# Performance work log

Measured on AMD Instinct MI355X. Metric: run time of the kernel, lower is better.

Reference implementation:

```python
import jax, jax.numpy as jnp
import numpy as np

B, T, P, H = 32, 4096, 512, 512  # batch, frames, phonemes, hidden


def setup_inputs() -> dict:
    key = jax.random.key(0)
    ks = jax.random.split(key, 10)
    encoder_out = jax.random.normal(ks[0], (B, P, H), dtype=jnp.float32)
    pitch = jax.random.normal(ks[1], (B, T), dtype=jnp.float32)
    beats = jax.random.normal(ks[2], (B, T), dtype=jnp.float32)
    align_phone = jnp.sort(jax.random.randint(ks[3], (B, T), 0, P, dtype=jnp.int32), axis=1)
    s = 1.0  # Linear(1,H) fan_in=1 init scale
    w_pitch = jax.random.uniform(ks[4], (H,), jnp.float32, -s, s)
    b_pitch = jax.random.uniform(ks[5], (H,), jnp.float32, -s, s)
    w_beats = jax.random.uniform(ks[6], (H,), jnp.float32, -s, s)
    b_beats = jax.random.uniform(ks[7], (H,), jnp.float32, -s, s)
    w_pos = jax.random.uniform(ks[8], (H,), jnp.float32, -s, s)
    b_pos = jax.random.uniform(ks[9], (H,), jnp.float32, -s, s)
    return {
        "encoder_out": encoder_out, "pitch": pitch, "beats": beats,
        "w_pitch": w_pitch, "b_pitch": b_pitch,
        "w_beats": w_beats, "b_beats": b_beats,
        "w_pos": w_pos, "b_pos": b_pos,
        "align_phone": align_phone,
    }


def _align(encoder_out, align_phone):
    # length-regulator: encoder index = running count of change points in align_phone
    Bn, Tn = align_phone.shape
    change = jnp.concatenate(
        [jnp.zeros((Bn, 1), jnp.int32),
         (align_phone[:, 1:] != align_phone[:, :-1]).astype(jnp.int32)], axis=1)
    idx = jnp.clip(jnp.cumsum(change, axis=1), 0, encoder_out.shape[1] - 1)  # [B,T]
    return jnp.take_along_axis(encoder_out, idx[:, :, None], axis=1)  # [B,T,H]


def reference(encoder_out, pitch, beats, w_pitch, b_pitch, w_beats, b_beats,
              w_pos, b_pos, align_phone):
    aligned = _align(encoder_out, align_phone)              # [B,T,H]
    out = aligned
    out = out + (pitch[..., None] * w_pitch + b_pitch)      # fc_pitch
    out = out + (beats[..., None] * w_beats + b_beats)      # fc_beats
    pos = jnp.arange(aligned.shape[1], dtype=aligned.dtype)[:, None]  # [T,1]
    out = out + (pos * w_pos + b_pos)                       # fc_pos on positions
    return out
```

## Files before the change

### kernel.cpp

```cpp
#include <hip/hip_runtime.h>

constexpr int B = 32;
constexpr int T = 4096;
constexpr int P = 512;
constexpr int H = 512;
constexpr int H4 = H / 4;
constexpr int LOG2_H4 = 7;

__global__ __launch_bounds__(256) void scan_idx_kernel(
    const int* __restrict__ align,
    const float* __restrict__ pitch,
    const float* __restrict__ beats,
    float4* __restrict__ packed) {
  const int b = blockIdx.x;
  const int tid = threadIdx.x;
  const long base = (long)b * T;
  constexpr int CH = T / 256;
  const int start = tid * CH;

  int local[CH];
  int prev = align[base + (start > 0 ? start - 1 : 0)];
  int run = 0;
#pragma unroll
  for (int j = 0; j < CH; ++j) {
    int a = align[base + start + j];
    run += ((start + j) > 0 && a != prev) ? 1 : 0;
    prev = a;
    local[j] = run;
  }

  __shared__ int sums[256];
  sums[tid] = run;
  __syncthreads();
  for (int off = 1; off < 256; off <<= 1) {
    int v = (tid >= off) ? sums[tid - off] : 0;
    __syncthreads();
    sums[tid] += v;
    __syncthreads();
  }
  const int excl = (tid > 0) ? sums[tid - 1] : 0;

#pragma unroll
  for (int j = 0; j < CH; ++j) {
    int v = excl + local[j];
    v = (v > (P - 1)) ? (P - 1) : v;
    float4 pk;
    pk.x = __int_as_float((b * P + v) << LOG2_H4);
    pk.y = pitch[base + start + j];
    pk.z = beats[base + start + j];
    pk.w = (float)(start + j);
    packed[base + start + j] = pk;
  }
}

__global__ __launch_bounds__(256) void fuse_kernel(
    const float4* __restrict__ enc,
    const float4* __restrict__ packed,
    const float4* __restrict__ wp, const float4* __restrict__ bp,
    const float4* __restrict__ wb, const float4* __restrict__ bb,
    const float4* __restrict__ wpos, const float4* __restrict__ bpos,
    float4* __restrict__ out) {
  const int tid = threadIdx.x;
  const int col = tid & (H4 - 1);
  const int rowHalf = tid >> 7;

  const float4 w1 = wp[col], w2 = wb[col], w3 = wpos[col];
  float4 cs;
  {
    const float4 c1 = bp[col], c2 = bb[col], c3 = bpos[col];
    cs.x = c1.x + c2.x + c3.x;
    cs.y = c1.y + c2.y + c3.y;
    cs.z = c1.z + c2.z + c3.z;
    cs.w = c1.w + c2.w + c3.w;
  }

  const int bid = blockIdx.x;
  const int xcd = bid & 7;
  const int lb = bid >> 3;
  constexpr int ROWS_PER_XCD = (B * T) / 8;
  int r = xcd * ROWS_PER_XCD + lb * 2 + rowHalf;
  const int rEnd = xcd * ROWS_PER_XCD + ROWS_PER_XCD;

  for (; r < rEnd; r += 512) {
    const int rU = __builtin_amdgcn_readfirstlane(r);
    const float4 pk = packed[rU];
    const int ebase = __float_as_int(pk.x);
    const float4 ev = enc[ebase + col];

    float4 o;
    o.x = ev.x + fmaf(pk.y, w1.x, fmaf(pk.z, w2.x, fmaf(pk.w, w3.x, cs.x)));
    o.y = ev.y + fmaf(pk.y, w1.y, fmaf(pk.z, w2.y, fmaf(pk.w, w3.y, cs.y)));
    o.z = ev.z + fmaf(pk.y, w1.z, fmaf(pk.z, w2.z, fmaf(pk.w, w3.z, cs.z)));
    o.w = ev.w + fmaf(pk.y, w1.w, fmaf(pk.z, w2.w, fmaf(pk.w, w3.w, cs.w)));

    out[((long)r << LOG2_H4) + col] = o;
  }
}

extern "C" void kernel_launch(void* const* d_in, const int* in_sizes, int n_in,
                              void* d_out, int out_size, void* d_ws, size_t ws_size,
                              hipStream_t stream) {
  const float* enc     = (const float*)d_in[0];
  const float* pitch   = (const float*)d_in[1];
  const float* beats   = (const float*)d_in[2];
  const float* w_pitch = (const float*)d_in[3];
  const float* b_pitch = (const float*)d_in[4];
  const float* w_beats = (const float*)d_in[5];
  const float* b_beats = (const float*)d_in[6];
  const float* w_pos   = (const float*)d_in[7];
  const float* b_pos   = (const float*)d_in[8];
  const int* align     = (const int*)d_in[9];

  float4* packed = (float4*)d_ws;

  scan_idx_kernel<<<B, 256, 0, stream>>>(align, pitch, beats, packed);

  fuse_kernel<<<2048, 256, 0, stream>>>(
      (const float4*)enc, packed,
      (const float4*)w_pitch, (const float4*)b_pitch,
      (const float4*)w_beats, (const float4*)b_beats,
      (const float4*)w_pos, (const float4*)b_pos,
      (float4*)d_out);
  (void)in_sizes; (void)n_in; (void)out_size; (void)ws_size;
}
```

Before: 329.3 us.

## Use contiguous 64-row blocks, dual-row loads, and nontemporal output stores

The persistent 2048-block grid with XCD-strided rows is replaced by 2048 blocks that each handle a contiguous 64-row chunk, with two rows loaded per iteration to raise memory-level parallelism. Output writes become nontemporal stores so the large write stream does not pollute cache, and the float4 code switches to native ext_vector types. The grid size is unchanged but the row-to-block mapping differs, so XCD-local L2 reuse of encoder rows may change. The fma ordering also changes slightly.

```diff
diff --git a/kernel.cpp b/kernel.cpp
--- a/kernel.cpp
+++ b/kernel.cpp
@@ -7,11 +7,13 @@
 constexpr int H4 = H / 4;
 constexpr int LOG2_H4 = 7;
 
+using f32x4 = __attribute__((ext_vector_type(4))) float;
+
 __global__ __launch_bounds__(256) void scan_idx_kernel(
     const int* __restrict__ align,
     const float* __restrict__ pitch,
     const float* __restrict__ beats,
-    float4* __restrict__ packed) {
+    f32x4* __restrict__ packed) {
   const int b = blockIdx.x;
   const int tid = threadIdx.x;
   const long base = (long)b * T;
@@ -44,7 +46,7 @@
   for (int j = 0; j < CH; ++j) {
     int v = excl + local[j];
     v = (v > (P - 1)) ? (P - 1) : v;
-    float4 pk;
+    f32x4 pk;
     pk.x = __int_as_float((b * P + v) << LOG2_H4);
     pk.y = pitch[base + start + j];
     pk.z = beats[base + start + j];
@@ -54,46 +56,37 @@
 }
 
 __global__ __launch_bounds__(256) void fuse_kernel(
-    const float4* __restrict__ enc,
-    const float4* __restrict__ packed,
-    const float4* __restrict__ wp, const float4* __restrict__ bp,
-    const float4* __restrict__ wb, const float4* __restrict__ bb,
-    const float4* __restrict__ wpos, const float4* __restrict__ bpos,
-    float4* __restrict__ out) {
+    const f32x4* __restrict__ enc,
+    const f32x4* __restrict__ packed,
+    const f32x4* __restrict__ wp, const f32x4* __restrict__ bp,
+    const f32x4* __restrict__ wb, const f32x4* __restrict__ bb,
+    const f32x4* __restrict__ wpos, const f32x4* __restrict__ bpos,
+    f32x4* __restrict__ out) {
   const int tid = threadIdx.x;
   const int col = tid & (H4 - 1);
   const int rowHalf = tid >> 7;
 
-  const float4 w1 = wp[col], w2 = wb[col], w3 = wpos[col];
-  float4 cs;
-  {
-    const float4 c1 = bp[col], c2 = bb[col], c3 = bpos[col];
-    cs.x = c1.x + c2.x + c3.x;
-    cs.y = c1.y + c2.y + c3.y;
-    cs.z = c1.z + c2.z + c3.z;
-    cs.w = c1.w + c2.w + c3.w;
-  }
+  const f32x4 w1 = wp[col], w2 = wb[col], w3 = wpos[col];
+  const f32x4 cs = bp[col] + bb[col] + bpos[col];
 
-  const int bid = blockIdx.x;
-  const int xcd = bid & 7;
-  const int lb = bid >> 3;
-  constexpr int ROWS_PER_XCD = (B * T) / 8;
-  int r = xcd * ROWS_PER_XCD + lb * 2 + rowHalf;
-  const int rEnd = xcd * ROWS_PER_XCD + ROWS_PER_XCD;
+  const int base = blockIdx.x * 64;
 
-  for (; r < rEnd; r += 512) {
-    const int rU = __builtin_amdgcn_readfirstlane(r);
-    const float4 pk = packed[rU];
-    const int ebase = __float_as_int(pk.x);
-    const float4 ev = enc[ebase + col];
+#pragma unroll 4
+  for (int i = 0; i < 16; ++i) {
+    const int ra = base + i * 4 + rowHalf;
+    const int rb = ra + 2;
+    const int raU = __builtin_amdgcn_readfirstlane(ra);
+    const int rbU = __builtin_amdgcn_readfirstlane(rb);
+    const f32x4 pka = packed[raU];
+    const f32x4 pkb = packed[rbU];
+    const f32x4 eva = enc[__float_as_int(pka.x) + col];
+    const f32x4 evb = enc[__float_as_int(pkb.x) + col];
 
-    float4 o;
-    o.x = ev.x + fmaf(pk.y, w1.x, fmaf(pk.z, w2.x, fmaf(pk.w, w3.x, cs.x)));
-    o.y = ev.y + fmaf(pk.y, w1.y, fmaf(pk.z, w2.y, fmaf(pk.w, w3.y, cs.y)));
-    o.z = ev.z + fmaf(pk.y, w1.z, fmaf(pk.z, w2.z, fmaf(pk.w, w3.z, cs.z)));
-    o.w = ev.w + fmaf(pk.y, w1.w, fmaf(pk.z, w2.w, fmaf(pk.w, w3.w, cs.w)));
+    const f32x4 oa = eva + pka.y * w1 + pka.z * w2 + pka.w * w3 + cs;
+    const f32x4 ob = evb + pkb.y * w1 + pkb.z * w2 + pkb.w * w3 + cs;
 
-    out[((long)r << LOG2_H4) + col] = o;
+    __builtin_nontemporal_store(oa, &out[((long)ra << LOG2_H4) + col]);
+    __builtin_nontemporal_store(ob, &out[((long)rb << LOG2_H4) + col]);
   }
 }
 
@@ -111,15 +104,15 @@
   const float* b_pos   = (const float*)d_in[8];
   const int* align     = (const int*)d_in[9];
 
-  float4* packed = (float4*)d_ws;
+  f32x4* packed = (f32x4*)d_ws;
 
   scan_idx_kernel<<<B, 256, 0, stream>>>(align, pitch, beats, packed);
 
-  fuse_kernel<<<2048, 256, 0, stream>>>(
-      (const float4*)enc, packed,
-      (const float4*)w_pitch, (const float4*)b_pitch,
-      (const float4*)w_beats, (const float4*)b_beats,
-      (const float4*)w_pos, (const float4*)b_pos,
-      (float4*)d_out);
+  fuse_kernel<<<(B * T) / 64, 256, 0, stream>>>(
+      (const f32x4*)enc, packed,
+      (const f32x4*)w_pitch, (const f32x4*)b_pitch,
+      (const f32x4*)w_beats, (const f32x4*)b_beats,
+      (const f32x4*)w_pos, (const f32x4*)b_pos,
+      (f32x4*)d_out);
   (void)in_sizes; (void)n_in; (void)out_size; (void)ws_size;
 }
```

Result: faster. 317.8 us (-3.5%).
